# Performance work log

Hardware: AMD Instinct MI355X
Metric: run time of the kernel (lower is better)

The kernel has to match this reference:

```python
import jax, jax.numpy as jnp
import numpy as np

NUM_HEADS = 2

def mha(q, k, v, w_in, b_in, w_out, b_out):
    # torch nn.MultiheadAttention with batch_first=True, packed in_proj
    E = q.shape[-1]
    Dh = E // NUM_HEADS
    wq, wk, wv = jnp.split(w_in, 3, axis=0)
    bq, bk, bv = jnp.split(b_in, 3, axis=0)
    qh = (q @ wq.T + bq).reshape(q.shape[0], q.shape[1], NUM_HEADS, Dh)
    kh = (k @ wk.T + bk).reshape(k.shape[0], k.shape[1], NUM_HEADS, Dh)
    vh = (v @ wv.T + bv).reshape(v.shape[0], v.shape[1], NUM_HEADS, Dh)
    scores = jnp.einsum('blhd,bmhd->bhlm', qh, kh) / jnp.sqrt(jnp.asarray(Dh, q.dtype))
    attn = jax.nn.softmax(scores, axis=-1)
    ctx = jnp.einsum('bhlm,bmhd->blhd', attn, vh).reshape(q.shape[0], q.shape[1], E)
    return ctx @ w_out.T + b_out


def setup_inputs() -> dict:
    key = jax.random.key(0)
    ks = jax.random.split(key, 10)
    B, S, F, E, H = 16384, 512, 4, 8, 16
    s = 0.3
    return {
        'x': jax.random.normal(ks[0], (B, S, E), jnp.float32),
        'Q': jax.random.normal(ks[1], (F, E), jnp.float32) * s,
        'sa_w_in': jax.random.normal(ks[2], (3 * E, E), jnp.float32) * s,
        'sa_b_in': jnp.zeros((3 * E,), jnp.float32),
        'sa_w_out': jax.random.normal(ks[3], (E, E), jnp.float32) * s,
        'sa_b_out': jnp.zeros((E,), jnp.float32),
        'ca_w_in': jax.random.normal(ks[4], (3 * E, E), jnp.float32) * s,
        'ca_b_in': jnp.zeros((3 * E,), jnp.float32),
        'ca_w_out': jax.random.normal(ks[5], (E, E), jnp.float32) * s,
        'ca_b_out': jnp.zeros((E,), jnp.float32),
        'r_w1': jax.random.normal(ks[6], (H, F * E), jnp.float32) * s,
        'r_b1': jnp.zeros((H,), jnp.float32),
        'r_w2': jax.random.normal(ks[7], (1, H), jnp.float32) * s,
        'r_b2': jnp.zeros((1,), jnp.float32),
    }


def reference(x, Q, sa_w_in, sa_b_in, sa_w_out, sa_b_out,
              ca_w_in, ca_b_in, ca_w_out, ca_b_out,
              r_w1, r_b1, r_w2, r_b2):
    B = x.shape[0]
    # self-attention over the (batch-identical) factor queries
    Qb = jnp.broadcast_to(Q[None], (B,) + Q.shape)  # [B, F, E]
    Q_upd = mha(Qb, Qb, Qb, sa_w_in, sa_b_in, sa_w_out, sa_b_out)
    # cross-attention: factors attend over the input sequence
    Q_cross = mha(Q_upd, x, x, ca_w_in, ca_b_in, ca_w_out, ca_b_out)  # [B, F, E]
    similarity = jnp.einsum('bfe,bse->bfs', Q_cross, x)  # [B, F, S]
    attn_weights = jax.nn.softmax(similarity, axis=-1)
    final_factors = jnp.einsum('bfs,bse->bfe', attn_weights, x)  # [B, F, E]
    fused = final_factors.reshape(B, -1)  # [B, F*E]
    h = jax.nn.relu(fused @ r_w1.T + r_b1)
    out = h @ r_w2.T + r_b2  # [B, 1]
    return out, similarity
```

## Files before the change

### kernel.cpp

```cpp
#include <hip/hip_runtime.h>

#define SEQ 512
#define EMB 8
#define NFAC 4

__global__ void precompute_kernel(
    const float* __restrict__ Q,
    const float* __restrict__ sa_w_in, const float* __restrict__ sa_b_in,
    const float* __restrict__ sa_w_out, const float* __restrict__ sa_b_out,
    const float* __restrict__ ca_w_in, const float* __restrict__ ca_b_in,
    float* __restrict__ ws)
{
    if (threadIdx.x != 0 || blockIdx.x != 0) return;
    float qh[4][8], kh[4][8], vh[4][8];
    for (int l = 0; l < 4; ++l)
        for (int j = 0; j < 8; ++j) {
            float aq = sa_b_in[j], ak = sa_b_in[8 + j], av = sa_b_in[16 + j];
            for (int e = 0; e < 8; ++e) {
                float q = Q[l * 8 + e];
                aq += q * sa_w_in[j * 8 + e];
                ak += q * sa_w_in[(8 + j) * 8 + e];
                av += q * sa_w_in[(16 + j) * 8 + e];
            }
            qh[l][j] = aq; kh[l][j] = ak; vh[l][j] = av;
        }
    float ctxf[4][8];
    for (int h = 0; h < 2; ++h)
        for (int l = 0; l < 4; ++l) {
            float sc[4];
            float mx = -1e30f;
            for (int m = 0; m < 4; ++m) {
                float a = 0.f;
                for (int d = 0; d < 4; ++d) a += qh[l][h*4+d] * kh[m][h*4+d];
                sc[m] = 0.5f * a;
                mx = fmaxf(mx, sc[m]);
            }
            float ssum = 0.f;
            for (int m = 0; m < 4; ++m) { sc[m] = __expf(sc[m] - mx); ssum += sc[m]; }
            for (int d = 0; d < 4; ++d) {
                float a = 0.f;
                for (int m = 0; m < 4; ++m) a += sc[m] * vh[m][h*4+d];
                ctxf[l][h*4+d] = a / ssum;
            }
        }
    float Qu[4][8];
    for (int l = 0; l < 4; ++l)
        for (int e2 = 0; e2 < 8; ++e2) {
            float a = sa_b_out[e2];
            for (int e = 0; e < 8; ++e) a += ctxf[l][e] * sa_w_out[e2 * 8 + e];
            Qu[l][e2] = a;
        }
    float qc[4][8];
    for (int l = 0; l < 4; ++l)
        for (int j = 0; j < 8; ++j) {
            float a = ca_b_in[j];
            for (int e = 0; e < 8; ++e) a += Qu[l][e] * ca_w_in[j * 8 + e];
            qc[l][j] = a;
        }
    for (int h = 0; h < 2; ++h)
        for (int f = 0; f < 4; ++f) {
            int p = h * 4 + f;
            for (int e = 0; e < 8; ++e) {
                float a = 0.f;
                for (int d = 0; d < 4; ++d) a += qc[f][h*4+d] * ca_w_in[(8 + h*4+d) * 8 + e];
                ws[p * 8 + e] = 0.5f * a;
            }
            float a = 0.f;
            for (int d = 0; d < 4; ++d) a += qc[f][h*4+d] * ca_b_in[8 + h*4+d];
            ws[64 + p] = 0.5f * a;
        }
}

__global__ __launch_bounds__(256, 2) void fused_kernel(
    const float* __restrict__ x,
    const float* __restrict__ ca_w_in, const float* __restrict__ ca_b_in,
    const float* __restrict__ ca_w_out, const float* __restrict__ ca_b_out,
    const float* __restrict__ r_w1, const float* __restrict__ r_b1,
    const float* __restrict__ r_w2, const float* __restrict__ r_b2,
    const float* __restrict__ ws,
    float* __restrict__ out, float* __restrict__ sim_out)
{
    const int b = blockIdx.x;
    const int tid = threadIdx.x;
    const int w = __builtin_amdgcn_readfirstlane(tid >> 6);
    const int lane = tid & 63;

    __shared__ float4 sctx4[8];
    __shared__ float sff[4][8];

    const float* xb = x + (size_t)b * (SEQ * EMB);

    const int p0 = 2 * w, p1 = 2 * w + 1;
    const int h = w >> 1;
    float wq0[8], wq1[8], wvv[4][8], bv[4];
    #pragma unroll
    for (int e = 0; e < 8; ++e) { wq0[e] = ws[p0 * 8 + e]; wq1[e] = ws[p1 * 8 + e]; }
    const float cb0 = ws[64 + p0], cb1 = ws[64 + p1];
    #pragma unroll
    for (int d = 0; d < 4; ++d) {
        bv[d] = ca_b_in[16 + h * 4 + d];
        #pragma unroll
        for (int e = 0; e < 8; ++e) wvv[d][e] = ca_w_in[(16 + h * 4 + d) * 8 + e];
    }

    float xr[8][8];
    float acc0[4] = {0.f, 0.f, 0.f, 0.f}, acc1[4] = {0.f, 0.f, 0.f, 0.f};
    float sum0 = 0.f, sum1 = 0.f;
    #pragma unroll
    for (int j = 0; j < 8; ++j) {
        const int s = lane + 64 * j;
        const float4* xp = (const float4*)(xb + s * 8);
        float4 lo = xp[0], hi = xp[1];
        xr[j][0] = lo.x; xr[j][1] = lo.y; xr[j][2] = lo.z; xr[j][3] = lo.w;
        xr[j][4] = hi.x; xr[j][5] = hi.y; xr[j][6] = hi.z; xr[j][7] = hi.w;
        float sc0 = cb0, sc1 = cb1;
        #pragma unroll
        for (int e = 0; e < 8; ++e) { sc0 += wq0[e] * xr[j][e]; sc1 += wq1[e] * xr[j][e]; }
        float e0 = __expf(sc0), e1 = __expf(sc1);
        sum0 += e0; sum1 += e1;
        #pragma unroll
        for (int d = 0; d < 4; ++d) {
            float vh = bv[d];
            #pragma unroll
            for (int e = 0; e < 8; ++e) vh += wvv[d][e] * xr[j][e];
            acc0[d] += e0 * vh;
            acc1[d] += e1 * vh;
        }
    }
    #pragma unroll
    for (int m = 1; m < 64; m <<= 1) {
        sum0 += __shfl_xor(sum0, m, 64);
        sum1 += __shfl_xor(sum1, m, 64);
        #pragma unroll
        for (int d = 0; d < 4; ++d) {
            acc0[d] += __shfl_xor(acc0[d], m, 64);
            acc1[d] += __shfl_xor(acc1[d], m, 64);
        }
    }
    if (lane == 0) {
        float i0 = 1.f / sum0, i1 = 1.f / sum1;
        sctx4[p0] = make_float4(acc0[0] * i0, acc0[1] * i0, acc0[2] * i0, acc0[3] * i0);
        sctx4[p1] = make_float4(acc1[0] * i1, acc1[1] * i1, acc1[2] * i1, acc1[3] * i1);
    }
    __syncthreads();

    float4 c0 = sctx4[w];
    float4 c1 = sctx4[4 + w];
    float qcr[8];
    #pragma unroll
    for (int e = 0; e < 8; ++e) {
        qcr[e] = ca_b_out[e]
            + c0.x * ca_w_out[e*8+0] + c0.y * ca_w_out[e*8+1]
            + c0.z * ca_w_out[e*8+2] + c0.w * ca_w_out[e*8+3]
            + c1.x * ca_w_out[e*8+4] + c1.y * ca_w_out[e*8+5]
            + c1.z * ca_w_out[e*8+6] + c1.w * ca_w_out[e*8+7];
    }

    float facc[8] = {0.f,0.f,0.f,0.f,0.f,0.f,0.f,0.f};
    float fsum = 0.f;
    float* simb = sim_out + (size_t)b * (NFAC * SEQ) + w * SEQ;
    #pragma unroll
    for (int j = 0; j < 8; ++j) {
        const int s = lane + 64 * j;
        float sim = 0.f;
        #pragma unroll
        for (int e = 0; e < 8; ++e) sim += qcr[e] * xr[j][e];
        simb[s] = sim;
        float ez = __expf(sim);
        fsum += ez;
        #pragma unroll
        for (int e = 0; e < 8; ++e) facc[e] += ez * xr[j][e];
    }
    #pragma unroll
    for (int m = 1; m < 64; m <<= 1) {
        fsum += __shfl_xor(fsum, m, 64);
        #pragma unroll
        for (int e = 0; e < 8; ++e) facc[e] += __shfl_xor(facc[e], m, 64);
    }
    if (lane == 0) {
        float inv = 1.f / fsum;
        #pragma unroll
        for (int e = 0; e < 8; ++e) sff[w][e] = facc[e] * inv;
    }
    __syncthreads();

    if (tid < 16) {
        float a = r_b1[tid];
        const float* fusedp = &sff[0][0];
        const float4* w1p = (const float4*)(r_w1 + tid * 32);
        #pragma unroll
        for (int k = 0; k < 8; ++k) {
            float4 ww = w1p[k];
            a += ww.x * fusedp[4*k+0] + ww.y * fusedp[4*k+1]
               + ww.z * fusedp[4*k+2] + ww.w * fusedp[4*k+3];
        }
        a = fmaxf(a, 0.f);
        float v = a * r_w2[tid];
        v += __shfl_xor(v, 1, 64);
        v += __shfl_xor(v, 2, 64);
        v += __shfl_xor(v, 4, 64);
        v += __shfl_xor(v, 8, 64);
        if (tid == 0) out[b] = v + r_b2[0];
    }
}

extern "C" void kernel_launch(void* const* d_in, const int* in_sizes, int n_in,
                              void* d_out, int out_size, void* d_ws, size_t ws_size,
                              hipStream_t stream) {
    const float* x        = (const float*)d_in[0];
    const float* Q        = (const float*)d_in[1];
    const float* sa_w_in  = (const float*)d_in[2];
    const float* sa_b_in  = (const float*)d_in[3];
    const float* sa_w_out = (const float*)d_in[4];
    const float* sa_b_out = (const float*)d_in[5];
    const float* ca_w_in  = (const float*)d_in[6];
    const float* ca_b_in  = (const float*)d_in[7];
    const float* ca_w_out = (const float*)d_in[8];
    const float* ca_b_out = (const float*)d_in[9];
    const float* r_w1     = (const float*)d_in[10];
    const float* r_b1     = (const float*)d_in[11];
    const float* r_w2     = (const float*)d_in[12];
    const float* r_b2     = (const float*)d_in[13];

    float* out = (float*)d_out;
    const int B = in_sizes[0] / (SEQ * EMB);
    float* sim = out + B;
    float* ws  = (float*)d_ws;

    precompute_kernel<<<1, 64, 0, stream>>>(Q, sa_w_in, sa_b_in, sa_w_out, sa_b_out,
                                            ca_w_in, ca_b_in, ws);
    fused_kernel<<<B, 256, 0, stream>>>(x, ca_w_in, ca_b_in, ca_w_out, ca_b_out,
                                        r_w1, r_b1, r_w2, r_b2, ws, out, sim);
}
```

Measured before the change: 464.9 us.

## Map one batch per wavefront and fold V/out projections into exp-weighted x sums

Each wavefront now handles a whole batch element, so a block covers four batches. Every wave accumulates exp-weighted sums of raw x for all eight query-head pairs, and the precomputed product of the output and value projections turns those sums into the cross-attention output. This removes the per-position V projection, the block-wide __syncthreads and the repeated global x reads. Reductions use DPP instead of shuffles, weights are packed into the workspace and read as uniform values, and launch bounds go to three blocks per CU. The risk is higher register pressure from the 64 per-lane accumulators, and relying on s_waitcnt instead of a barrier for intra-wave LDS ordering.

Measured after the change: 559.5 us. +20.4%, slower.

```diff
diff --git a/kernel.cpp b/kernel.cpp
--- a/kernel.cpp
+++ b/kernel.cpp
@@ -3,15 +3,24 @@
 #define SEQ 512
 #define EMB 8
 #define NFAC 4
+
 
 __global__ void precompute_kernel(
     const float* __restrict__ Q,
     const float* __restrict__ sa_w_in, const float* __restrict__ sa_b_in,
     const float* __restrict__ sa_w_out, const float* __restrict__ sa_b_out,
     const float* __restrict__ ca_w_in, const float* __restrict__ ca_b_in,
+    const float* __restrict__ ca_w_out, const float* __restrict__ ca_b_out,
+    const float* __restrict__ r_w1, const float* __restrict__ r_b1,
+    const float* __restrict__ r_w2, const float* __restrict__ r_b2,
     float* __restrict__ ws)
 {
-    if (threadIdx.x != 0 || blockIdx.x != 0) return;
+    const int tid = threadIdx.x;
+    for (int k = tid; k < 512; k += 64) ws[208 + k] = r_w1[k];
+    if (tid < 16) { ws[720 + tid] = r_b1[tid]; ws[736 + tid] = r_w2[tid]; }
+    if (tid != 0) return;
+    ws[752] = r_b2[0];
+
     float qh[4][8], kh[4][8], vh[4][8];
     for (int l = 0; l < 4; ++l)
         for (int j = 0; j < 8; ++j) {
@@ -69,138 +78,182 @@
             for (int d = 0; d < 4; ++d) a += qc[f][h*4+d] * ca_b_in[8 + h*4+d];
             ws[64 + p] = 0.5f * a;
         }
-}
-
-__global__ __launch_bounds__(256, 2) void fused_kernel(
-    const float* __restrict__ x,
-    const float* __restrict__ ca_w_in, const float* __restrict__ ca_b_in,
-    const float* __restrict__ ca_w_out, const float* __restrict__ ca_b_out,
-    const float* __restrict__ r_w1, const float* __restrict__ r_b1,
-    const float* __restrict__ r_w2, const float* __restrict__ r_b2,
-    const float* __restrict__ ws,
+    for (int h = 0; h < 2; ++h)
+        for (int e = 0; e < 8; ++e)
+            for (int e2 = 0; e2 < 8; ++e2) {
+                float a = 0.f;
+                for (int d = 0; d < 4; ++d)
+                    a += ca_w_out[e*8 + h*4+d] * ca_w_in[(16 + h*4+d)*8 + e2];
+                ws[72 + h*64 + e*8 + e2] = a;
+            }
+    for (int e = 0; e < 8; ++e) {
+        float a = ca_b_out[e];
+        for (int hd = 0; hd < 8; ++hd) a += ca_w_out[e*8 + hd] * ca_b_in[16 + hd];
+        ws[200 + e] = a;
+    }
+}
+
+__device__ __forceinline__ float wave_sum64(float v) {
+    v += __int_as_float(__builtin_amdgcn_update_dpp(0, __float_as_int(v), 0x111, 0xf, 0xf, true));
+    v += __int_as_float(__builtin_amdgcn_update_dpp(0, __float_as_int(v), 0x112, 0xf, 0xf, true));
+    v += __int_as_float(__builtin_amdgcn_update_dpp(0, __float_as_int(v), 0x114, 0xf, 0xf, true));
+    v += __int_as_float(__builtin_amdgcn_update_dpp(0, __float_as_int(v), 0x118, 0xf, 0xf, true));
+    v += __int_as_float(__builtin_amdgcn_update_dpp(0, __float_as_int(v), 0x142, 0xa, 0xf, true));
+    v += __int_as_float(__builtin_amdgcn_update_dpp(0, __float_as_int(v), 0x143, 0xc, 0xf, true));
+    return v;
+}
+__device__ __forceinline__ float row16_sum(float v) {
+    v += __int_as_float(__builtin_amdgcn_update_dpp(0, __float_as_int(v), 0x111, 0xf, 0xf, true));
+    v += __int_as_float(__builtin_amdgcn_update_dpp(0, __float_as_int(v), 0x112, 0xf, 0xf, true));
+    v += __int_as_float(__builtin_amdgcn_update_dpp(0, __float_as_int(v), 0x114, 0xf, 0xf, true));
+    v += __int_as_float(__builtin_amdgcn_update_dpp(0, __float_as_int(v), 0x118, 0xf, 0xf, true));
+    return v;
+}
+
+__device__ __forceinline__ float uload(const float* p) {
+    return __int_as_float(__builtin_amdgcn_readfirstlane(__float_as_int(*p)));
+}
+
+__global__ __launch_bounds__(256, 3) void fused_kernel(
+    const float* __restrict__ x, const float* __restrict__ ws,
     float* __restrict__ out, float* __restrict__ sim_out)
 {
-    const int b = blockIdx.x;
     const int tid = threadIdx.x;
     const int w = __builtin_amdgcn_readfirstlane(tid >> 6);
     const int lane = tid & 63;
-
-    __shared__ float4 sctx4[8];
-    __shared__ float sff[4][8];
+    const int b = blockIdx.x * 4 + w;
+
+    __shared__ float sX[4][72];
+    __shared__ float sQ[4][32];
+    __shared__ float sF[4][32];
 
     const float* xb = x + (size_t)b * (SEQ * EMB);
 
-    const int p0 = 2 * w, p1 = 2 * w + 1;
-    const int h = w >> 1;
-    float wq0[8], wq1[8], wvv[4][8], bv[4];
-    #pragma unroll
-    for (int e = 0; e < 8; ++e) { wq0[e] = ws[p0 * 8 + e]; wq1[e] = ws[p1 * 8 + e]; }
-    const float cb0 = ws[64 + p0], cb1 = ws[64 + p1];
-    #pragma unroll
-    for (int d = 0; d < 4; ++d) {
-        bv[d] = ca_b_in[16 + h * 4 + d];
-        #pragma unroll
-        for (int e = 0; e < 8; ++e) wvv[d][e] = ca_w_in[(16 + h * 4 + d) * 8 + e];
-    }
-
-    float xr[8][8];
-    float acc0[4] = {0.f, 0.f, 0.f, 0.f}, acc1[4] = {0.f, 0.f, 0.f, 0.f};
-    float sum0 = 0.f, sum1 = 0.f;
+    float4 lo[8], hi[8];
     #pragma unroll
     for (int j = 0; j < 8; ++j) {
-        const int s = lane + 64 * j;
-        const float4* xp = (const float4*)(xb + s * 8);
-        float4 lo = xp[0], hi = xp[1];
-        xr[j][0] = lo.x; xr[j][1] = lo.y; xr[j][2] = lo.z; xr[j][3] = lo.w;
-        xr[j][4] = hi.x; xr[j][5] = hi.y; xr[j][6] = hi.z; xr[j][7] = hi.w;
-        float sc0 = cb0, sc1 = cb1;
-        #pragma unroll
-        for (int e = 0; e < 8; ++e) { sc0 += wq0[e] * xr[j][e]; sc1 += wq1[e] * xr[j][e]; }
-        float e0 = __expf(sc0), e1 = __expf(sc1);
-        sum0 += e0; sum1 += e1;
-        #pragma unroll
-        for (int d = 0; d < 4; ++d) {
-            float vh = bv[d];
-            #pragma unroll
-            for (int e = 0; e < 8; ++e) vh += wvv[d][e] * xr[j][e];
-            acc0[d] += e0 * vh;
-            acc1[d] += e1 * vh;
-        }
-    }
-    #pragma unroll
-    for (int m = 1; m < 64; m <<= 1) {
-        sum0 += __shfl_xor(sum0, m, 64);
-        sum1 += __shfl_xor(sum1, m, 64);
-        #pragma unroll
-        for (int d = 0; d < 4; ++d) {
-            acc0[d] += __shfl_xor(acc0[d], m, 64);
-            acc1[d] += __shfl_xor(acc1[d], m, 64);
-        }
-    }
-    if (lane == 0) {
-        float i0 = 1.f / sum0, i1 = 1.f / sum1;
-        sctx4[p0] = make_float4(acc0[0] * i0, acc0[1] * i0, acc0[2] * i0, acc0[3] * i0);
-        sctx4[p1] = make_float4(acc1[0] * i1, acc1[1] * i1, acc1[2] * i1, acc1[3] * i1);
-    }
-    __syncthreads();
-
-    float4 c0 = sctx4[w];
-    float4 c1 = sctx4[4 + w];
-    float qcr[8];
-    #pragma unroll
-    for (int e = 0; e < 8; ++e) {
-        qcr[e] = ca_b_out[e]
-            + c0.x * ca_w_out[e*8+0] + c0.y * ca_w_out[e*8+1]
-            + c0.z * ca_w_out[e*8+2] + c0.w * ca_w_out[e*8+3]
-            + c1.x * ca_w_out[e*8+4] + c1.y * ca_w_out[e*8+5]
-            + c1.z * ca_w_out[e*8+6] + c1.w * ca_w_out[e*8+7];
-    }
-
-    float facc[8] = {0.f,0.f,0.f,0.f,0.f,0.f,0.f,0.f};
-    float fsum = 0.f;
-    float* simb = sim_out + (size_t)b * (NFAC * SEQ) + w * SEQ;
+        const float4* xp = (const float4*)(xb + (size_t)(lane + 64 * j) * EMB);
+        lo[j] = xp[0];
+        hi[j] = xp[1];
+    }
+
+    float wkq[8][8], csb[8];
+    #pragma unroll
+    for (int p = 0; p < 8; ++p) {
+        csb[p] = uload(ws + 64 + p);
+        #pragma unroll
+        for (int e = 0; e < 8; ++e) wkq[p][e] = uload(ws + p * 8 + e);
+    }
+
+    float Xa[8][8], Sa[8];
+    #pragma unroll
+    for (int p = 0; p < 8; ++p) {
+        Sa[p] = 0.f;
+        #pragma unroll
+        for (int e = 0; e < 8; ++e) Xa[p][e] = 0.f;
+    }
     #pragma unroll
     for (int j = 0; j < 8; ++j) {
-        const int s = lane + 64 * j;
-        float sim = 0.f;
-        #pragma unroll
-        for (int e = 0; e < 8; ++e) sim += qcr[e] * xr[j][e];
-        simb[s] = sim;
-        float ez = __expf(sim);
-        fsum += ez;
-        #pragma unroll
-        for (int e = 0; e < 8; ++e) facc[e] += ez * xr[j][e];
-    }
-    #pragma unroll
-    for (int m = 1; m < 64; m <<= 1) {
-        fsum += __shfl_xor(fsum, m, 64);
-        #pragma unroll
-        for (int e = 0; e < 8; ++e) facc[e] += __shfl_xor(facc[e], m, 64);
-    }
-    if (lane == 0) {
-        float inv = 1.f / fsum;
-        #pragma unroll
-        for (int e = 0; e < 8; ++e) sff[w][e] = facc[e] * inv;
-    }
-    __syncthreads();
-
-    if (tid < 16) {
-        float a = r_b1[tid];
-        const float* fusedp = &sff[0][0];
-        const float4* w1p = (const float4*)(r_w1 + tid * 32);
-        #pragma unroll
-        for (int k = 0; k < 8; ++k) {
-            float4 ww = w1p[k];
-            a += ww.x * fusedp[4*k+0] + ww.y * fusedp[4*k+1]
-               + ww.z * fusedp[4*k+2] + ww.w * fusedp[4*k+3];
-        }
-        a = fmaxf(a, 0.f);
-        float v = a * r_w2[tid];
-        v += __shfl_xor(v, 1, 64);
-        v += __shfl_xor(v, 2, 64);
-        v += __shfl_xor(v, 4, 64);
-        v += __shfl_xor(v, 8, 64);
-        if (tid == 0) out[b] = v + r_b2[0];
+        float xv[8] = {lo[j].x, lo[j].y, lo[j].z, lo[j].w,
+                       hi[j].x, hi[j].y, hi[j].z, hi[j].w};
+        float ep[8];
+        #pragma unroll
+        for (int p = 0; p < 8; ++p) {
+            float sc = csb[p];
+            #pragma unroll
+            for (int e = 0; e < 8; ++e) sc += wkq[p][e] * xv[e];
+            ep[p] = __expf(sc);
+            Sa[p] += ep[p];
+        }
+        #pragma unroll
+        for (int p = 0; p < 8; ++p)
+            #pragma unroll
+            for (int e = 0; e < 8; ++e) Xa[p][e] += ep[p] * xv[e];
+    }
+    #pragma unroll
+    for (int p = 0; p < 8; ++p) {
+        Sa[p] = wave_sum64(Sa[p]);
+        #pragma unroll
+        for (int e = 0; e < 8; ++e) Xa[p][e] = wave_sum64(Xa[p][e]);
+    }
+    if (lane == 63) {
+        #pragma unroll
+        for (int p = 0; p < 8; ++p) {
+            sX[w][64 + p] = Sa[p];
+            #pragma unroll
+            for (int e = 0; e < 8; ++e) sX[w][p * 8 + e] = Xa[p][e];
+        }
+    }
+    asm volatile("s_waitcnt lgkmcnt(0)" ::: "memory");
+
+    if (lane < 32) {
+        const int f = lane >> 3, e = lane & 7;
+        const float i0 = 1.f / sX[w][64 + f];
+        const float i1 = 1.f / sX[w][64 + 4 + f];
+        float d0 = 0.f, d1 = 0.f;
+        #pragma unroll
+        for (int e2 = 0; e2 < 8; ++e2) {
+            d0 += ws[72 + e * 8 + e2] * sX[w][f * 8 + e2];
+            d1 += ws[136 + e * 8 + e2] * sX[w][(4 + f) * 8 + e2];
+        }
+        sQ[w][f * 8 + e] = ws[200 + e] + d0 * i0 + d1 * i1;
+    }
+    asm volatile("s_waitcnt lgkmcnt(0)" ::: "memory");
+
+    float qc[4][8];
+    #pragma unroll
+    for (int f = 0; f < 4; ++f)
+        #pragma unroll
+        for (int e = 0; e < 8; ++e) qc[f][e] = sQ[w][f * 8 + e];
+
+    float ff[4][8], fz[4];
+    #pragma unroll
+    for (int f = 0; f < 4; ++f) {
+        fz[f] = 0.f;
+        #pragma unroll
+        for (int e = 0; e < 8; ++e) ff[f][e] = 0.f;
+    }
+    float* simb = sim_out + (size_t)b * (NFAC * SEQ);
+    #pragma unroll
+    for (int j = 0; j < 8; ++j) {
+        float xv[8] = {lo[j].x, lo[j].y, lo[j].z, lo[j].w,
+                       hi[j].x, hi[j].y, hi[j].z, hi[j].w};
+        #pragma unroll
+        for (int f = 0; f < 4; ++f) {
+            float s = 0.f;
+            #pragma unroll
+            for (int e = 0; e < 8; ++e) s += qc[f][e] * xv[e];
+            simb[f * SEQ + lane + 64 * j] = s;
+            float ez = __expf(s);
+            fz[f] += ez;
+            #pragma unroll
+            for (int e = 0; e < 8; ++e) ff[f][e] += ez * xv[e];
+        }
+    }
+    #pragma unroll
+    for (int f = 0; f < 4; ++f) {
+        fz[f] = wave_sum64(fz[f]);
+        #pragma unroll
+        for (int e = 0; e < 8; ++e) ff[f][e] = wave_sum64(ff[f][e]);
+    }
+    if (lane == 63) {
+        #pragma unroll
+        for (int f = 0; f < 4; ++f) {
+            float inv = 1.f / fz[f];
+            #pragma unroll
+            for (int e = 0; e < 8; ++e) sF[w][f * 8 + e] = ff[f][e] * inv;
+        }
+    }
+    asm volatile("s_waitcnt lgkmcnt(0)" ::: "memory");
+
+    if (lane < 16) {
+        float h = ws[720 + lane];
+        #pragma unroll
+        for (int k = 0; k < 32; ++k) h += ws[208 + lane * 32 + k] * sF[w][k];
+        h = fmaxf(h, 0.f);
+        float v = h * ws[736 + lane];
+        v = row16_sum(v);
+        if (lane == 15) out[b] = v + ws[752];
     }
 }
 
@@ -228,7 +281,7 @@
     float* ws  = (float*)d_ws;
 
     precompute_kernel<<<1, 64, 0, stream>>>(Q, sa_w_in, sa_b_in, sa_w_out, sa_b_out,
-                                            ca_w_in, ca_b_in, ws);
-    fused_kernel<<<B, 256, 0, stream>>>(x, ca_w_in, ca_b_in, ca_w_out, ca_b_out,
-                                        r_w1, r_b1, r_w2, r_b2, ws, out, sim);
-}
+                                            ca_w_in, ca_b_in, ca_w_out, ca_b_out,
+                                            r_w1, r_b1, r_w2, r_b2, ws);
+    fused_kernel<<<B / 4, 256, 0, stream>>>(x, ws, out, sim);
+}
```
